# Kernel optimization log

Measured on AMD Instinct MI355X. Metric: run time of the kernel, lower is better.

Reference implementation:

```python
import jax, jax.numpy as jnp
import numpy as np
import math

BS, L, NNF, NEF = 8, 107, 17, 9
NH, EH, H3, NL, K = 128, 32, 32, 10, 3
PC, TL, TH, FF, NCLS = 32, 3, 8, 256, 3
D = NH + PC
HD = D // TH
RPG = 150
N = BS * L
E = BS * (2 * (L - 1) + RPG)
EPS = 1e-5


def _ln(z, g, b):
    m = z.mean(-1, keepdims=True)
    v = ((z - m) ** 2).mean(-1, keepdims=True)
    return (z - m) / jnp.sqrt(v + EPS) * g + b


def _gelu(z):
    return jax.nn.gelu(z, approximate=False)


def _forward(x, edge_attr, cheb_w, cheb_b, ee_w, ee_b, mlp_w1, mlp_b1, mlp_w2, mlp_b2,
             root_w, conv_b, ln_g, ln_b, attn_in_w, attn_in_b, attn_out_w, attn_out_b,
             ff_w1, ff_b1, ff_w2, ff_b2, tln1_g, tln1_b, tln2_g, tln2_b, lin_w, lin_b,
             seq_edge_index, edge_index):
    n = x.shape[0]
    # --- ChebConv (K=3, sym norm, lambda_max=2 -> L_hat = -D^-1/2 A D^-1/2) on seq edges ---
    ss, sd = seq_edge_index[0], seq_edge_index[1]
    deg = jax.ops.segment_sum(jnp.ones_like(ss, dtype=x.dtype), ss, num_segments=n)
    dinv = jnp.where(deg > 0, jax.lax.rsqrt(jnp.maximum(deg, 1e-12)), 0.0)
    w = -(dinv[ss] * dinv[sd])
    lap = lambda h: jax.ops.segment_sum(w[:, None] * h[ss], sd, num_segments=n)
    tx1 = lap(x)
    tx2 = 2.0 * lap(tx1) - x
    h = x @ cheb_w[0] + tx1 @ cheb_w[1] + tx2 @ cheb_w[2] + cheb_b

    # --- edge encoder ---
    ea = edge_attr @ ee_w + ee_b
    src, dst = edge_index[0], edge_index[1]

    # --- NNConv: per-edge weight W_e = MLP(ea) in R^{NHxNH}; gather-matmul-scatter ---
    def nnconv(h, l):
        we = ((ea @ mlp_w1[l] + mlp_b1[l]) @ mlp_w2[l] + mlp_b2[l]).reshape(-1, NH, NH)
        msg = jnp.einsum('ei,eio->eo', h[src], we)
        return jax.ops.segment_sum(msg, dst, num_segments=n) + h @ root_w[l] + conv_b[l]

    h = nnconv(h, 0)  # layers[0].conv applied directly (no residual)
    for l in range(1, NL):  # DeepGCNLayer res+: x + conv(gelu(LN(x)))
        h = h + nnconv(_gelu(_ln(h, ln_g[l], ln_b[l])), l)
    h = _gelu(_ln(h, ln_g[0], ln_b[0]))  # reuses layer 0's norm/act

    # --- sinusoidal position encoding (dim=PC), concat ---
    p = jnp.arange(L, dtype=x.dtype)[:, None]
    div = jnp.exp(jnp.arange(0, PC, 2, dtype=x.dtype) * (-math.log(10000.0) / PC))
    pos = jnp.zeros((L, PC), dtype=x.dtype)
    pos = pos.at[:, 0::2].set(jnp.sin(p * div)).at[:, 1::2].set(jnp.cos(p * div))

    t = jnp.concatenate([h.reshape(BS, L, NH), jnp.broadcast_to(pos, (BS, L, PC))], -1)

    # --- post-norm TransformerEncoder (relu FFN), vectorized over graphs ---
    scale = 1.0 / math.sqrt(HD)
    for l in range(TL):
        qkv = t @ attn_in_w[l] + attn_in_b[l]
        q, k, v = jnp.split(qkv, 3, axis=-1)
        q = q.reshape(BS, L, TH, HD)
        k = k.reshape(BS, L, TH, HD)
        v = v.reshape(BS, L, TH, HD)
        a = jax.nn.softmax(jnp.einsum('bqhd,bkhd->bhqk', q, k) * scale, axis=-1)
        o = jnp.einsum('bhqk,bkhd->bqhd', a, v).reshape(BS, L, D) @ attn_out_w[l] + attn_out_b[l]
        t = _ln(t + o, tln1_g[l], tln1_b[l])
        f = jax.nn.relu(t @ ff_w1[l] + ff_b1[l]) @ ff_w2[l] + ff_b2[l]
        t = _ln(t + f, tln2_g[l], tln2_b[l])

    return t.reshape(n, D) @ lin_w + lin_b


def setup_inputs():
    rng = np.random.default_rng(0)
    ks = iter(jax.random.split(jax.random.key(0), 40))
    # bidirectional sequence edges per graph + random pair edges
    base = np.arange(L - 1)
    s = np.concatenate([base, base + 1])
    d = np.concatenate([base + 1, base])
    off = (np.arange(BS) * L)[:, None]
    seq_src = (s[None] + off).ravel()
    seq_dst = (d[None] + off).ravel()
    r_src = (rng.integers(0, L, (BS, RPG)) + off).ravel()
    r_dst = (rng.integers(0, L, (BS, RPG)) + off).ravel()
    edge_index = jnp.asarray(np.stack([np.concatenate([seq_src, r_src]),
                                       np.concatenate([seq_dst, r_dst])]), dtype=jnp.int32)
    seq_edge_index = jnp.asarray(np.stack([seq_src, seq_dst]), dtype=jnp.int32)
    n_seq = seq_src.shape[0]

    def nrm(shape, sc=0.05):
        return jax.random.normal(next(ks), shape, dtype=jnp.float32) * sc

    x = jax.random.normal(next(ks), (N, NNF), dtype=jnp.float32)
    edge_attr = jax.random.normal(next(ks), (E, NEF), dtype=jnp.float32)
    col0 = jnp.concatenate([jnp.zeros((n_seq,), jnp.float32), jnp.ones((E - n_seq,), jnp.float32)])
    edge_attr = edge_attr.at[:, 0].set(col0)
    return {
        'x': x, 'edge_attr': edge_attr,
        'cheb_w': nrm((K, NNF, NH), 0.1), 'cheb_b': nrm((NH,), 0.02),
        'ee_w': nrm((NEF, EH), 0.1), 'ee_b': nrm((EH,), 0.02),
        'mlp_w1': nrm((NL, EH, H3), 0.1), 'mlp_b1': nrm((NL, H3), 0.02),
        'mlp_w2': nrm((NL, H3, NH * NH), 0.01), 'mlp_b2': nrm((NL, NH * NH), 0.01),
        'root_w': nrm((NL, NH, NH), 0.05), 'conv_b': nrm((NL, NH), 0.02),
        'ln_g': jnp.ones((NL, NH), jnp.float32), 'ln_b': jnp.zeros((NL, NH), jnp.float32),
        'attn_in_w': nrm((TL, D, 3 * D), 0.05), 'attn_in_b': nrm((TL, 3 * D), 0.02),
        'attn_out_w': nrm((TL, D, D), 0.05), 'attn_out_b': nrm((TL, D), 0.02),
        'ff_w1': nrm((TL, D, FF), 0.05), 'ff_b1': nrm((TL, FF), 0.02),
        'ff_w2': nrm((TL, FF, D), 0.05), 'ff_b2': nrm((TL, D), 0.02),
        'tln1_g': jnp.ones((TL, D), jnp.float32), 'tln1_b': jnp.zeros((TL, D), jnp.float32),
        'tln2_g': jnp.ones((TL, D), jnp.float32), 'tln2_b': jnp.zeros((TL, D), jnp.float32),
        'lin_w': nrm((D, NCLS), 0.05), 'lin_b': nrm((NCLS,), 0.02),
        'seq_edge_index': seq_edge_index, 'edge_index': edge_index,
    }


def reference(x, edge_attr, cheb_w, cheb_b, ee_w, ee_b, mlp_w1, mlp_b1, mlp_w2, mlp_b2,
              root_w, conv_b, ln_g, ln_b, attn_in_w, attn_in_b, attn_out_w, attn_out_b,
              ff_w1, ff_b1, ff_w2, ff_b2, tln1_g, tln1_b, tln2_g, tln2_b, lin_w, lin_b,
              seq_edge_index, edge_index):
    return _forward(x, edge_attr, cheb_w, cheb_b, ee_w, ee_b, mlp_w1, mlp_b1, mlp_w2, mlp_b2,
                    root_w, conv_b, ln_g, ln_b, attn_in_w, attn_in_b, attn_out_w, attn_out_b,
                    ff_w1, ff_b1, ff_w2, ff_b2, tln1_g, tln1_b, tln2_g, tln2_b, lin_w, lin_b,
                    seq_edge_index, edge_index)
```

## Files before the change

### kernel.cpp

```cpp
#include <hip/hip_runtime.h>
#include <hip/hip_bf16.h>
#include <math.h>

#define BSZ   8
#define LSEQ  107
#define NNF   17
#define NEF   9
#define NH    128
#define EHD   32
#define H3D   32
#define NLAY  10
#define PCD   32
#define TLAY  3
#define THD   8
#define FFD   256
#define NCLS  3
#define DD    160
#define HDD   20
#define NND   856
#define NPAD  896
#define NE    2896
#define CSTR  32
#define QKVP  512
#define PRJP  192
#define KTOT  1408
#define ALD2  1416

#define SB_CHEB 428
#define SB_PAD  (SB_CHEB)
#define SB_CSR1 (SB_PAD + 1)
#define SB_TPK  (SB_CSR1 + 1)
#define NTPK    171
#define SB_BIAS (SB_TPK + NTPK)
#define SB_WT   (SB_BIAS + 1)
#define NWT     160
#define SB_TOT  (SB_WT + NWT)

typedef __bf16 bf16;
typedef __bf16 bf16x2 __attribute__((ext_vector_type(2)));
typedef __bf16 bf16x8 __attribute__((ext_vector_type(8)));
typedef float  f32x4  __attribute__((ext_vector_type(4)));

__device__ __forceinline__ float geluf(float z) {
    return 0.5f * z * (1.0f + erff(z * 0.70710678118654752f));
}
__device__ __forceinline__ float wred(float v) {
    #pragma unroll
    for (int o = 32; o; o >>= 1) v += __shfl_xor(v, o, 64);
    return v;
}
__device__ __forceinline__ float dinv_path(int n) {
    return (n == 0 || n == LSEQ - 1) ? 1.0f : 0.70710678118654752f;
}

__global__ __launch_bounds__(256) void k_setup(
        const float* __restrict__ x, const float* __restrict__ cw,
        const float* __restrict__ cb, bf16* __restrict__ zA, bf16* __restrict__ zB,
        const float* __restrict__ eattr, const float* __restrict__ eew,
        const float* __restrict__ eeb, const float* __restrict__ w1,
        const float* __restrict__ b1,
        const float* __restrict__ w2, const float* __restrict__ b2,
        const float* __restrict__ rootw, bf16* __restrict__ bpk,
        const int* __restrict__ ei, int* __restrict__ deg,
        int* __restrict__ csrs, float* __restrict__ csrw,
        const float* __restrict__ ain_w, const float* __restrict__ aow,
        const float* __restrict__ ffw1, const float* __restrict__ ffw2,
        const float* __restrict__ ain_b, const float* __restrict__ aob,
        const float* __restrict__ ffb1, const float* __restrict__ ffb2,
        bf16* __restrict__ bqkv, bf16* __restrict__ bproj,
        bf16* __restrict__ bff1, bf16* __restrict__ bff2,
        float* __restrict__ tb_bias) {
    __shared__ __align__(16) char sm[24576];
    int blk = blockIdx.x, tid = threadIdx.x;
    if (blk < SB_CHEB) {
        float (*xs)[5][NNF] = (float (*)[5][NNF])sm;
        int s = tid >> 7, o = tid & 127;
        int n = blk * 2 + s;
        int g = n / LSEQ, i = n - g * LSEQ;
        if (o < 5 * NNF) {
            int k = o / NNF, f = o - k * NNF;
            int p = i - 2 + k; p = p < 0 ? 0 : (p > LSEQ - 1 ? LSEQ - 1 : p);
            xs[s][k][f] = x[(g * LSEQ + p) * NNF + f];
        }
        __syncthreads();
        float di  = dinv_path(i);
        float dm1 = dinv_path(i - 1 < 0 ? 0 : i - 1);
        float dp1 = dinv_path(i + 1 > LSEQ - 1 ? LSEQ - 1 : i + 1);
        float dm2 = dinv_path(i - 2 < 0 ? 0 : i - 2);
        float dp2 = dinv_path(i + 2 > LSEQ - 1 ? LSEQ - 1 : i + 2);
        float wmc = (i > 0)        ? -(dm1 * di) : 0.f;
        float wpc = (i < LSEQ - 1) ? -(dp1 * di) : 0.f;
        float wmm = (i - 1 > 0)        ? -(dm2 * dm1) : 0.f;
        float wpm = -(di * dm1);
        float wmp = -(di * dp1);
        float wpp = (i + 1 < LSEQ - 1) ? -(dp2 * dp1) : 0.f;
        float acc = cb[o];
        #pragma unroll
        for (int f = 0; f < NNF; ++f) {
            float xm2 = xs[s][0][f], xm1 = xs[s][1][f], x0 = xs[s][2][f],
                  xp1 = xs[s][3][f], xp2 = xs[s][4][f];
            float t1c = wmc * xm1 + wpc * xp1;
            float t1m = wmm * xm2 + wpm * x0;
            float t1p = wmp * x0 + wpp * xp2;
            float t2 = 2.f * (wmc * t1m + wpc * t1p) - x0;
            acc += x0 * cw[f * NH + o] + t1c * cw[(NNF + f) * NH + o]
                 + t2 * cw[(2 * NNF + f) * NH + o];
        }
        zA[n * NH + o] = (bf16)acc;
    } else if (blk == SB_PAD) {
        for (int i = tid; i < (NPAD - NND) * NH; i += 256) {
            zA[NND * NH + i] = (bf16)0.f;
            zB[NND * NH + i] = (bf16)0.f;
        }
    } else if (blk == SB_CSR1) {
        int* ldeg = (int*)sm;
        for (int i = tid; i < NND; i += 256) ldeg[i] = 0;
        __syncthreads();
        for (int e = tid; e < NE; e += 256) {
            int d = ei[NE + e];
            int slot = atomicAdd(&ldeg[d], 1);
            if (slot < CSTR) {
                int idx = d * CSTR + slot;
                csrs[idx] = ei[e];
                float* wp = csrw + (size_t)idx * 10;
                #pragma unroll
                for (int f = 0; f < NEF; ++f) wp[f] = eattr[e * NEF + f];
                wp[9] = 1.0f;
            }
        }
        __syncthreads();
        for (int i = tid; i < NND; i += 256) deg[i] = ldeg[i];
    } else if (blk < SB_BIAS) {
        bf16 (*tt)[65] = (bf16 (*)[65])sm;
        int v = blk - SB_TPK;
        int tl = v / 57, t = v % 57;
        const float* src; bf16* dst; int Kd, srcN, ct, kt;
        if (t < 24)      { ct = t & 7;  kt = t >> 3;          src = ain_w + (size_t)tl * DD * 3 * DD; srcN = 3 * DD; Kd = DD;  dst = bqkv  + (size_t)tl * QKVP * DD; }
        else if (t < 33) { int u = t - 24; ct = u % 3; kt = u / 3; src = aow + (size_t)tl * DD * DD;  srcN = DD;     Kd = DD;  dst = bproj + (size_t)tl * PRJP * DD; }
        else if (t < 45) { int u = t - 33; ct = u % 4; kt = u / 4; src = ffw1 + (size_t)tl * DD * FFD; srcN = FFD;   Kd = DD;  dst = bff1  + (size_t)tl * FFD * DD; }
        else             { int u = t - 45; ct = u % 3; kt = u / 3; src = ffw2 + (size_t)tl * FFD * DD; srcN = DD;    Kd = FFD; dst = bff2  + (size_t)tl * PRJP * FFD; }
        int cc = tid & 63, rr = tid >> 6;
        #pragma unroll
        for (int rep = 0; rep < 16; ++rep) {
            int kl = rep * 4 + rr;
            int k = kt * 64 + kl;
            int col = ct * 64 + cc;
            float val = (k < Kd && col < srcN) ? src[(size_t)k * srcN + col] : 0.f;
            tt[kl][cc] = (bf16)val;
        }
        __syncthreads();
        int k = kt * 64 + cc;
        if (k < Kd) {
            #pragma unroll
            for (int rep = 0; rep < 16; ++rep) {
                int c = rep * 4 + rr;
                dst[(size_t)(ct * 64 + c) * Kd + k] = tt[cc][c];
            }
        }
    } else if (blk == SB_BIAS) {
        for (int i = tid; i < 3 * 1152; i += 256) {
            int tl = i / 1152, r = i % 1152;
            float val;
            if (r < 512)      { val = (r < 480) ? ain_b[tl * 480 + r] : 0.f; }
            else if (r < 704) { int c = r - 512; val = (c < 160) ? aob[tl * 160 + c] : 0.f; }
            else if (r < 960) { int c = r - 704; val = ffb1[tl * 256 + c]; }
            else              { int c = r - 960; val = (c < 160) ? ffb2[tl * 160 + c] : 0.f; }
            tb_bias[i] = val;
        }
    } else {
        float* gw  = (float*)sm;
        bf16* ldsT = (bf16*)(sm + 2048);
        int v = blk - SB_WT;
        int l = v >> 4, chunk = v & 15;
        int io0 = chunk * 1024;
        for (int e = tid; e < 320; e += 256) {
            int f = e >> 5, j = e & 31;
            float acc;
            if (f < 9) {
                acc = 0.f;
                for (int m = 0; m < EHD; ++m)
                    acc += eew[f * EHD + m] * w1[(size_t)l * EHD * H3D + m * H3D + j];
            } else {
                acc = b1[l * H3D + j];
                for (int m = 0; m < EHD; ++m)
                    acc += eeb[m] * w1[(size_t)l * EHD * H3D + m * H3D + j];
            }
            gw[e] = acc;
        }
        __syncthreads();
        int io = io0 + tid * 4;
        const float* w2l = w2 + (size_t)l * 524288;
        float acc[10][4];
        float4 b2v = *(const float4*)(b2 + (size_t)l * 16384 + io);
        #pragma unroll
        for (int f = 0; f < 9; ++f) { acc[f][0] = 0.f; acc[f][1] = 0.f; acc[f][2] = 0.f; acc[f][3] = 0.f; }
        acc[9][0] = b2v.x; acc[9][1] = b2v.y; acc[9][2] = b2v.z; acc[9][3] = b2v.w;
        for (int j = 0; j < H3D; ++j) {
            float4 wv4 = *(const float4*)(w2l + (size_t)j * 16384 + io);
            #pragma unroll
            for (int f = 0; f < 10; ++f) {
                float gf = gw[f * 32 + j];
                acc[f][0] += gf * wv4.x; acc[f][1] += gf * wv4.y;
                acc[f][2] += gf * wv4.z; acc[f][3] += gf * wv4.w;
            }
        }
        int o4 = (tid & 31) * 4, il = tid >> 5;
        #pragma unroll
        for (int f = 0; f < 10; ++f)
            #pragma unroll
            for (int k = 0; k < 4; ++k)
                ldsT[(f * 128 + o4 + k) * 8 + il] = (bf16)acc[f][k];
        float4 rv = *(const float4*)(rootw + (size_t)l * 16384 + io);
        ldsT[(10 * 128 + o4 + 0) * 8 + il] = (bf16)rv.x;
        ldsT[(10 * 128 + o4 + 1) * 8 + il] = (bf16)rv.y;
        ldsT[(10 * 128 + o4 + 2) * 8 + il] = (bf16)rv.z;
        ldsT[(10 * 128 + o4 + 3) * 8 + il] = (bf16)rv.w;
        __syncthreads();
        if (tid < 128) {
            int o = tid;
            bf16* dst = bpk + (size_t)l * 128 * KTOT + (size_t)o * KTOT + chunk * 8;
            #pragma unroll
            for (int f = 0; f < 11; ++f) {
                bf16x8 val = *(bf16x8*)(ldsT + ((size_t)f * 128 + o) * 8);
                *(bf16x8*)(dst + f * 128) = val;
            }
        }
    }
}

__global__ __launch_bounds__(512) void k_layer(const bf16* __restrict__ zin,
                                               float* __restrict__ h,
                                               const bf16* __restrict__ bpkL,
                                               const float* __restrict__ conv_b,
                                               const float* __restrict__ lng,
                                               const float* __restrict__ lnb,
                                               bf16* __restrict__ zout,
                                               float* __restrict__ tbuf,
                                               const int* __restrict__ deg,
                                               const int* __restrict__ csrs,
                                               const float* __restrict__ csrw,
                                               int l) {
    __shared__ bf16 As[16][ALD2];
    __shared__ float outs[16][128];
    int tid = threadIdx.x, lane = tid & 63, wv = tid >> 6;
    int r0 = blockIdx.x * 16;
    for (int rr = 0; rr < 2; ++rr) {
        int r = wv * 2 + rr;
        int d = r0 + r;
        float acc[10][2];
        #pragma unroll
        for (int f = 0; f < 10; ++f) { acc[f][0] = 0.f; acc[f][1] = 0.f; }
        int dg = 0;
        if (d < NND) { dg = deg[d]; if (dg > CSTR) dg = CSTR; }
        for (int k = 0; k < dg; ++k) {
            int idx = d * CSTR + k;
            int s = csrs[idx];
            bf16x2 zz = *(const bf16x2*)(zin + (size_t)s * NH + 2 * lane);
            float z0 = (float)zz[0], z1 = (float)zz[1];
            const float* ww = csrw + (size_t)idx * 10;
            #pragma unroll
            for (int f = 0; f < 10; ++f) {
                float wf = ww[f];
                acc[f][0] += wf * z0;
                acc[f][1] += wf * z1;
            }
        }
        #pragma unroll
        for (int f = 0; f < 10; ++f) {
            bf16x2 av; av[0] = (bf16)acc[f][0]; av[1] = (bf16)acc[f][1];
            *(bf16x2*)(&As[r][f * 128 + 2 * lane]) = av;
        }
        bf16x2 zr = *(const bf16x2*)(zin + (size_t)d * NH + 2 * lane);
        *(bf16x2*)(&As[r][1280 + 2 * lane]) = zr;
    }
    __syncthreads();
    {
        int rA = lane & 15, q = lane >> 4, q8 = q * 8;
        const bf16* Af = &As[rA][0];
        const bf16* B0 = bpkL + (size_t)(wv * 16 + rA) * KTOT;
        f32x4 zf = {0.f, 0.f, 0.f, 0.f};
        f32x4 aA = zf, aB = zf;
        #pragma unroll 2
        for (int ks = 0; ks < 22; ++ks) {
            int kb = ks * 32 + q8;
            bf16x8 av = *(const bf16x8*)(Af + kb);
            bf16x8 b0 = *(const bf16x8*)(B0 + kb);
            aA = __builtin_amdgcn_mfma_f32_16x16x32_bf16(av, b0, aA, 0, 0, 0);
        }
        #pragma unroll 2
        for (int ks = 22; ks < 44; ++ks) {
            int kb = ks * 32 + q8;
            bf16x8 av = *(const bf16x8*)(Af + kb);
            bf16x8 b0 = *(const bf16x8*)(B0 + kb);
            aB = __builtin_amdgcn_mfma_f32_16x16x32_bf16(av, b0, aB, 0, 0, 0);
        }
        #pragma unroll
        for (int reg = 0; reg < 4; ++reg)
            outs[q * 4 + reg][wv * 16 + rA] = aA[reg] + aB[reg];
    }
    __syncthreads();
    for (int rr = 0; rr < 2; ++rr) {
        int r = wv * 2 + rr;
        int d = r0 + r;
        if (d >= NND) {
            if (l < NLAY - 1) {
                zout[d * NH + lane] = (bf16)0.f;
                zout[d * NH + lane + 64] = (bf16)0.f;
            }
            continue;
        }
        float v0 = outs[r][lane] + conv_b[l * NH + lane];
        float v1 = outs[r][lane + 64] + conv_b[l * NH + lane + 64];
        if (l > 0) {
            v0 += h[d * NH + lane];
            v1 += h[d * NH + lane + 64];
        }
        if (l < NLAY - 1) {
            h[d * NH + lane] = v0;
            h[d * NH + lane + 64] = v1;
        }
        float m = wred(v0 + v1) * (1.f / NH);
        float d0 = v0 - m, d1 = v1 - m;
        float var = wred(d0 * d0 + d1 * d1) * (1.f / NH);
        float rs = rsqrtf(var + 1e-5f);
        if (l < NLAY - 1) {
            int ln = l + 1;
            zout[d * NH + lane] = (bf16)geluf(d0 * rs * lng[ln * NH + lane] + lnb[ln * NH + lane]);
            zout[d * NH + lane + 64] = (bf16)geluf(d1 * rs * lng[ln * NH + lane + 64] + lnb[ln * NH + lane + 64]);
        } else {
            tbuf[(size_t)d * DD + lane] = geluf(d0 * rs * lng[lane] + lnb[lane]);
            tbuf[(size_t)d * DD + lane + 64] = geluf(d1 * rs * lng[lane + 64] + lnb[lane + 64]);
        }
    }
    if (l == NLAY - 1) {
        for (int idx = tid; idx < 16 * PCD; idx += 512) {
            int r = idx >> 5, pc = idx & 31;
            int d = r0 + r;
            if (d < NND) {
                int qq = d % LSEQ;
                float twoi = (float)(pc & ~1);
                float ang = (float)qq * expf(-twoi * 0.28782313662425572f);
                tbuf[(size_t)d * DD + NH + pc] = (pc & 1) ? cosf(ang) : sinf(ang);
            }
        }
    }
}

__global__ __launch_bounds__(256) void k_gmm(const float* __restrict__ A,
                                             const bf16* __restrict__ bp,
                                             const float* __restrict__ biasP,
                                             float* __restrict__ C,
                                             int ksteps, int K, int PW, int act) {
    int lane = threadIdx.x & 63, wv = threadIdx.x >> 6;
    int m0 = blockIdx.y * 64 + wv * 16;
    int ct = blockIdx.x;
    int r = lane & 15, q = lane >> 4, q8 = q * 8;
    const float* Arow = A + (size_t)(m0 + r) * K;
    const bf16* Bb = bp + ((size_t)ct * 64 + r) * K;
    f32x4 a0 = {0.f,0.f,0.f,0.f}, a1 = a0, a2 = a0, a3 = a0;
    for (int ks = 0; ks < ksteps; ++ks) {
        int kb = ks * 32 + q8;
        float4 f0 = *(const float4*)(Arow + kb);
        float4 f1 = *(const float4*)(Arow + kb + 4);
        bf16x8 av;
        av[0] = (bf16)f0.x; av[1] = (bf16)f0.y; av[2] = (bf16)f0.z; av[3] = (bf16)f0.w;
        av[4] = (bf16)f1.x; av[5] = (bf16)f1.y; av[6] = (bf16)f1.z; av[7] = (bf16)f1.w;
        bf16x8 b0 = *(const bf16x8*)(Bb + 0 * 16 * K + kb);
        bf16x8 b1 = *(const bf16x8*)(Bb + 1 * 16 * K + kb);
        bf16x8 b2 = *(const bf16x8*)(Bb + 2 * 16 * K + kb);
        bf16x8 b3 = *(const bf16x8*)(Bb + 3 * 16 * K + kb);
        a0 = __builtin_amdgcn_mfma_f32_16x16x32_bf16(av, b0, a0, 0, 0, 0);
        a1 = __builtin_amdgcn_mfma_f32_16x16x32_bf16(av, b1, a1, 0, 0, 0);
        a2 = __builtin_amdgcn_mfma_f32_16x16x32_bf16(av, b2, a2, 0, 0, 0);
        a3 = __builtin_amdgcn_mfma_f32_16x16x32_bf16(av, b3, a3, 0, 0, 0);
    }
    int cb = ct * 64;
    #pragma unroll
    for (int reg = 0; reg < 4; ++reg) {
        float* Crow = C + (size_t)(m0 + q * 4 + reg) * PW + cb;
        float v0 = a0[reg] + biasP[cb + 0 * 16 + r];
        float v1 = a1[reg] + biasP[cb + 1 * 16 + r];
        float v2 = a2[reg] + biasP[cb + 2 * 16 + r];
        float v3 = a3[reg] + biasP[cb + 3 * 16 + r];
        if (act) { v0 = fmaxf(v0, 0.f); v1 = fmaxf(v1, 0.f); v2 = fmaxf(v2, 0.f); v3 = fmaxf(v3, 0.f); }
        Crow[0 * 16 + r] = v0;
        Crow[1 * 16 + r] = v1;
        Crow[2 * 16 + r] = v2;
        Crow[3 * 16 + r] = v3;
    }
}

__global__ __launch_bounds__(512) void k_pln(const float* __restrict__ A,
                                             const bf16* __restrict__ bp,
                                             const float* __restrict__ biasP,
                                             int ksteps, int K,
                                             float* __restrict__ t,
                                             const float* __restrict__ g,
                                             const float* __restrict__ bvec,
                                             int tail,
                                             const bf16* __restrict__ tbp,
                                             const float* __restrict__ tbias_,
                                             float* __restrict__ tout,
                                             const float* __restrict__ lw,
                                             const float* __restrict__ lb,
                                             float* __restrict__ outp) {
    __shared__ float outs[16][PRJP];
    __shared__ bf16 Als[16][176];
    int tid = threadIdx.x, lane = tid & 63, wv = tid >> 6;
    int m0 = blockIdx.x * 16;
    if (wv < 6) {
        int r = lane & 15, q = lane >> 4, q8 = q * 8;
        const float* Arow = A + (size_t)(m0 + r) * K;
        int cb0 = wv * 32;
        const bf16* B0 = bp + ((size_t)(cb0 + r) * K);
        const bf16* B1 = bp + ((size_t)(cb0 + 16 + r) * K);
        f32x4 a0 = {0.f,0.f,0.f,0.f}, a1 = a0;
        for (int ks = 0; ks < ksteps; ++ks) {
            int kb = ks * 32 + q8;
            float4 f0 = *(const float4*)(Arow + kb);
            float4 f1 = *(const float4*)(Arow + kb + 4);
            bf16x8 av;
            av[0] = (bf16)f0.x; av[1] = (bf16)f0.y; av[2] = (bf16)f0.z; av[3] = (bf16)f0.w;
            av[4] = (bf16)f1.x; av[5] = (bf16)f1.y; av[6] = (bf16)f1.z; av[7] = (bf16)f1.w;
            bf16x8 b0 = *(const bf16x8*)(B0 + kb);
            bf16x8 b1 = *(const bf16x8*)(B1 + kb);
            a0 = __builtin_amdgcn_mfma_f32_16x16x32_bf16(av, b0, a0, 0, 0, 0);
            a1 = __builtin_amdgcn_mfma_f32_16x16x32_bf16(av, b1, a1, 0, 0, 0);
        }
        #pragma unroll
        for (int reg = 0; reg < 4; ++reg) {
            int rw = q * 4 + reg;
            outs[rw][cb0 + r] = a0[reg] + biasP[cb0 + r];
            outs[rw][cb0 + 16 + r] = a1[reg] + biasP[cb0 + 16 + r];
        }
    }
    __syncthreads();
    for (int rr = 0; rr < 2; ++rr) {
        int r = wv * 2 + rr;
        int d = m0 + r;
        if (d >= NND) continue;
        int c0 = lane, c1 = lane + 64, c2 = lane + 128;
        float v0 = outs[r][c0] + t[(size_t)d * DD + c0];
        float v1 = outs[r][c1] + t[(size_t)d * DD + c1];
        float v2 = (lane < 32) ? (outs[r][c2] + t[(size_t)d * DD + c2]) : 0.f;
        float m = wred(v0 + v1 + v2) * (1.f / DD);
        float d0 = v0 - m, d1 = v1 - m, d2 = (lane < 32) ? (v2 - m) : 0.f;
        float var = wred(d0 * d0 + d1 * d1 + d2 * d2) * (1.f / DD);
        float rs = rsqrtf(var + 1e-5f);
        float n0 = d0 * rs * g[c0] + bvec[c0];
        float n1 = d1 * rs * g[c1] + bvec[c1];
        float n2 = (lane < 32) ? (d2 * rs * g[c2] + bvec[c2]) : 0.f;
        t[(size_t)d * DD + c0] = n0;
        t[(size_t)d * DD + c1] = n1;
        if (lane < 32) t[(size_t)d * DD + c2] = n2;
        Als[r][c0] = (bf16)n0;
        Als[r][c1] = (bf16)n1;
        if (lane < 32) Als[r][c2] = (bf16)n2;
        if (tail == 0 && outp) {
            #pragma unroll
            for (int cls = 0; cls < NCLS; ++cls) {
                float part = n0 * lw[c0 * NCLS + cls] + n1 * lw[c1 * NCLS + cls]
                           + ((lane < 32) ? n2 * lw[c2 * NCLS + cls] : 0.f);
                float tot = wred(part);
                if (lane == 0) outp[d * NCLS + cls] = tot + lb[cls];
            }
        }
    }
    if (!tail) return;
    __syncthreads();
    {
        int PW = (tail == 1) ? FFD : QKVP;
        int ntile = (tail == 1) ? 2 : 4;
        int rA = lane & 15, q = lane >> 4, q8 = q * 8;
        for (int ctl = 0; ctl < ntile; ++ctl) {
            int cb = (wv * ntile + ctl) * 16;
            const bf16* Bb = tbp + ((size_t)cb + rA) * DD;
            f32x4 a0 = {0.f,0.f,0.f,0.f};
            #pragma unroll
            for (int ks = 0; ks < 5; ++ks) {
                int kb = ks * 32 + q8;
                bf16x8 av = *(const bf16x8*)(&Als[rA][0] + kb);
                bf16x8 b0 = *(const bf16x8*)(Bb + kb);
                a0 = __builtin_amdgcn_mfma_f32_16x16x32_bf16(av, b0, a0, 0, 0, 0);
            }
            #pragma unroll
            for (int reg = 0; reg < 4; ++reg) {
                float* Crow = tout + (size_t)(m0 + q * 4 + reg) * PW + cb;
                float v0 = a0[reg] + tbias_[cb + rA];
                if (tail == 1) v0 = fmaxf(v0, 0.f);
                Crow[rA] = v0;
            }
        }
    }
}

#define UPD4(ac, V) { ac.x = ac.x * corr + p * V.x; ac.y = ac.y * corr + p * V.y; \
                      ac.z = ac.z * corr + p * V.z; ac.w = ac.w * corr + p * V.w; }
__global__ __launch_bounds__(64) void k_attn(const float* __restrict__ qkv,
                                             float* __restrict__ aout) {
    __shared__ float4 Ks4[LSEQ * 5], Vs4[LSEQ * 5];
    int bh = blockIdx.x;
    int b = bh >> 3, hh = bh & 7;
    int tid = threadIdx.x;
    for (int i = tid; i < LSEQ * 5; i += 64) {
        int kq = i / 5, c4 = i - kq * 5;
        const float* rowp = qkv + (size_t)(b * LSEQ + kq) * QKVP + hh * HDD;
        Ks4[i] = ((const float4*)(rowp + DD))[c4];
        Vs4[i] = ((const float4*)(rowp + 2 * DD))[c4];
    }
    __syncthreads();
    int q = blockIdx.y * 64 + tid;
    if (q >= LSEQ) return;
    const float4* qp = (const float4*)(qkv + (size_t)(b * LSEQ + q) * QKVP + hh * HDD);
    float4 q0 = qp[0], q1 = qp[1], q2 = qp[2], q3 = qp[3], q4 = qp[4];
    const float scale = 0.22360679774997896f;
    float mx = -3.0e38f, sum = 0.f;
    float4 z = {0.f, 0.f, 0.f, 0.f};
    float4 ac0 = z, ac1 = z, ac2 = z, ac3 = z, ac4 = z;
    for (int k = 0; k < LSEQ; ++k) {
        const float4* kp = Ks4 + k * 5;
        float4 K0 = kp[0], K1 = kp[1], K2 = kp[2], K3 = kp[3], K4 = kp[4];
        float a0 = q0.x * K0.x + q0.y * K0.y + q0.z * K0.z + q0.w * K0.w;
        float a1 = q1.x * K1.x + q1.y * K1.y + q1.z * K1.z + q1.w * K1.w;
        float a2 = q2.x * K2.x + q2.y * K2.y + q2.z * K2.z + q2.w * K2.w;
        float a3 = q3.x * K3.x + q3.y * K3.y + q3.z * K3.z + q3.w * K3.w;
        float a4 = q4.x * K4.x + q4.y * K4.y + q4.z * K4.z + q4.w * K4.w;
        float s = (((a0 + a1) + (a2 + a3)) + a4) * scale;
        float mn = fmaxf(mx, s);
        float corr = __expf(mx - mn);
        float p = __expf(s - mn);
        mx = mn;
        sum = sum * corr + p;
        const float4* vp = Vs4 + k * 5;
        float4 V0 = vp[0], V1 = vp[1], V2 = vp[2], V3 = vp[3], V4 = vp[4];
        UPD4(ac0, V0); UPD4(ac1, V1); UPD4(ac2, V2); UPD4(ac3, V3); UPD4(ac4, V4);
    }
    float inv = 1.f / sum;
    float4* op = (float4*)(aout + (size_t)(b * LSEQ + q) * DD + hh * HDD);
    float4 o0 = {ac0.x * inv, ac0.y * inv, ac0.z * inv, ac0.w * inv};
    float4 o1 = {ac1.x * inv, ac1.y * inv, ac1.z * inv, ac1.w * inv};
    float4 o2 = {ac2.x * inv, ac2.y * inv, ac2.z * inv, ac2.w * inv};
    float4 o3 = {ac3.x * inv, ac3.y * inv, ac3.z * inv, ac3.w * inv};
    float4 o4 = {ac4.x * inv, ac4.y * inv, ac4.z * inv, ac4.w * inv};
    op[0] = o0; op[1] = o1; op[2] = o2; op[3] = o3; op[4] = o4;
}

extern "C" void kernel_launch(void* const* d_in, const int* in_sizes, int n_in,
                              void* d_out, int out_size, void* d_ws, size_t ws_size,
                              hipStream_t stream) {
    (void)in_sizes; (void)n_in; (void)out_size; (void)ws_size;
    const float* x      = (const float*)d_in[0];
    const float* eattr  = (const float*)d_in[1];
    const float* cheb_w = (const float*)d_in[2];
    const float* cheb_b = (const float*)d_in[3];
    const float* ee_w   = (const float*)d_in[4];
    const float* ee_b   = (const float*)d_in[5];
    const float* mlp_w1 = (const float*)d_in[6];
    const float* mlp_b1 = (const float*)d_in[7];
    const float* mlp_w2 = (const float*)d_in[8];
    const float* mlp_b2 = (const float*)d_in[9];
    const float* root_w = (const float*)d_in[10];
    const float* conv_b = (const float*)d_in[11];
    const float* ln_g   = (const float*)d_in[12];
    const float* ln_b   = (const float*)d_in[13];
    const float* ain_w  = (const float*)d_in[14];
    const float* ain_b  = (const float*)d_in[15];
    const float* aow    = (const float*)d_in[16];
    const float* aob    = (const float*)d_in[17];
    const float* ffw1   = (const float*)d_in[18];
    const float* ffb1   = (const float*)d_in[19];
    const float* ffw2   = (const float*)d_in[20];
    const float* ffb2   = (const float*)d_in[21];
    const float* t1g    = (const float*)d_in[22];
    const float* t1b    = (const float*)d_in[23];
    const float* t2g    = (const float*)d_in[24];
    const float* t2b    = (const float*)d_in[25];
    const float* lin_w  = (const float*)d_in[26];
    const float* lin_b  = (const float*)d_in[27];
    const int* ei       = (const int*)d_in[29];

    char* w = (char*)d_ws;
    size_t off = 0;
    auto alloc = [&](size_t bytes) -> void* {
        void* p = w + off;
        off += (bytes + 255) & ~(size_t)255;
        return p;
    };
    bf16*  bpk   = (bf16*)alloc((size_t)NLAY * 128 * KTOT * 2);
    float* h     = (float*)alloc((size_t)NND * NH * 4);
    bf16*  zA    = (bf16*)alloc((size_t)NPAD * NH * 2);
    bf16*  zB    = (bf16*)alloc((size_t)NPAD * NH * 2);
    float* tbuf  = (float*)alloc((size_t)NPAD * DD * 4);
    float* qkvC  = (float*)alloc((size_t)NPAD * QKVP * 4);
    float* abuf  = (float*)alloc((size_t)NPAD * DD * 4);
    float* f1    = (float*)alloc((size_t)NPAD * FFD * 4);
    int*   deg   = (int*)alloc((size_t)NND * 4);
    int*   csrs  = (int*)alloc((size_t)NND * CSTR * 4);
    float* csrw  = (float*)alloc((size_t)NND * CSTR * 10 * 4);
    bf16*  bqkv  = (bf16*)alloc((size_t)TLAY * QKVP * DD * 2);
    bf16*  bproj = (bf16*)alloc((size_t)TLAY * PRJP * DD * 2);
    bf16*  bff1  = (bf16*)alloc((size_t)TLAY * FFD * DD * 2);
    bf16*  bff2  = (bf16*)alloc((size_t)TLAY * PRJP * FFD * 2);
    float* tbias = (float*)alloc((size_t)TLAY * 1152 * 4);

    k_setup<<<SB_TOT, 256, 0, stream>>>(x, cheb_w, cheb_b, zA, zB,
                                        eattr, ee_w, ee_b, mlp_w1, mlp_b1,
                                        mlp_w2, mlp_b2, root_w, bpk,
                                        ei, deg, csrs, csrw,
                                        ain_w, aow, ffw1, ffw2,
                                        ain_b, aob, ffb1, ffb2,
                                        bqkv, bproj, bff1, bff2, tbias);

    bf16* zcur = zA;
    bf16* znxt = zB;
    for (int l = 0; l < NLAY; ++l) {
        k_layer<<<NPAD / 16, 512, 0, stream>>>(zcur, h, bpk + (size_t)l * 128 * KTOT,
                                               conv_b, ln_g, ln_b, znxt, tbuf,
                                               deg, csrs, csrw, l);
        bf16* tmp = zcur; zcur = znxt; znxt = tmp;
    }

    k_gmm<<<dim3(QKVP / 64, 14), 256, 0, stream>>>(tbuf, bqkv, tbias, qkvC, 5, DD, QKVP, 0);
    for (int tl = 0; tl < TLAY; ++tl) {
        const float* bb = tbias + (size_t)tl * 1152;
        k_attn<<<dim3(BSZ * THD, 2), 64, 0, stream>>>(qkvC, abuf);
        k_pln<<<NPAD / 16, 512, 0, stream>>>(abuf, bproj + (size_t)tl * PRJP * DD, bb + 512,
                                             5, DD, tbuf,
                                             t1g + (size_t)tl * DD, t1b + (size_t)tl * DD,
                                             1, bff1 + (size_t)tl * FFD * DD, bb + 704, f1,
                                             nullptr, nullptr, nullptr);
        int last = (tl == TLAY - 1);
        k_pln<<<NPAD / 16, 512, 0, stream>>>(f1, bff2 + (size_t)tl * PRJP * FFD, bb + 960,
                                             8, FFD, tbuf,
                                             t2g + (size_t)tl * DD, t2b + (size_t)tl * DD,
                                             last ? 0 : 2,
                                             last ? nullptr : bqkv + (size_t)(tl + 1) * QKVP * DD,
                                             last ? nullptr : tbias + (size_t)(tl + 1) * 1152,
                                             last ? nullptr : qkvC,
                                             last ? lin_w : nullptr,
                                             last ? lin_b : nullptr,
                                             last ? (float*)d_out : nullptr);
    }
}
```

Measured before the change: 466.6 us.

## Double k_layer block to 1024 threads with one row per wave and split-K MFMA

Each k_layer block now runs 16 waves instead of 8. Each wave gathers one destination row instead of two, and the MFMA stage splits the 44 K-steps between two waves per 16-column tile. The two partial results are written to separate shared buffers and summed in the epilogue. This halves the serial gather and matmul work per wave and adds latency hiding, at the cost of more shared memory and register pressure under 1024-thread launch bounds.

```diff
diff --git a/kernel.cpp b/kernel.cpp
--- a/kernel.cpp
+++ b/kernel.cpp
@@ -228,24 +228,24 @@
     }
 }
 
-__global__ __launch_bounds__(512) void k_layer(const bf16* __restrict__ zin,
-                                               float* __restrict__ h,
-                                               const bf16* __restrict__ bpkL,
-                                               const float* __restrict__ conv_b,
-                                               const float* __restrict__ lng,
-                                               const float* __restrict__ lnb,
-                                               bf16* __restrict__ zout,
-                                               float* __restrict__ tbuf,
-                                               const int* __restrict__ deg,
-                                               const int* __restrict__ csrs,
-                                               const float* __restrict__ csrw,
-                                               int l) {
+__global__ __launch_bounds__(1024) void k_layer(const bf16* __restrict__ zin,
+                                                float* __restrict__ h,
+                                                const bf16* __restrict__ bpkL,
+                                                const float* __restrict__ conv_b,
+                                                const float* __restrict__ lng,
+                                                const float* __restrict__ lnb,
+                                                bf16* __restrict__ zout,
+                                                float* __restrict__ tbuf,
+                                                const int* __restrict__ deg,
+                                                const int* __restrict__ csrs,
+                                                const float* __restrict__ csrw,
+                                                int l) {
     __shared__ bf16 As[16][ALD2];
-    __shared__ float outs[16][128];
+    __shared__ float outs[2][16][128];
     int tid = threadIdx.x, lane = tid & 63, wv = tid >> 6;
     int r0 = blockIdx.x * 16;
-    for (int rr = 0; rr < 2; ++rr) {
-        int r = wv * 2 + rr;
+    {
+        int r = wv;
         int d = r0 + r;
         float acc[10][2];
         #pragma unroll
@@ -276,64 +276,58 @@
     __syncthreads();
     {
         int rA = lane & 15, q = lane >> 4, q8 = q * 8;
+        int ct = wv >> 1, kh = wv & 1;
         const bf16* Af = &As[rA][0];
-        const bf16* B0 = bpkL + (size_t)(wv * 16 + rA) * KTOT;
-        f32x4 zf = {0.f, 0.f, 0.f, 0.f};
-        f32x4 aA = zf, aB = zf;
+        const bf16* B0 = bpkL + (size_t)(ct * 16 + rA) * KTOT;
+        f32x4 aA = {0.f, 0.f, 0.f, 0.f};
+        int ks0 = kh * 22;
         #pragma unroll 2
         for (int ks = 0; ks < 22; ++ks) {
-            int kb = ks * 32 + q8;
+            int kb = (ks0 + ks) * 32 + q8;
             bf16x8 av = *(const bf16x8*)(Af + kb);
             bf16x8 b0 = *(const bf16x8*)(B0 + kb);
             aA = __builtin_amdgcn_mfma_f32_16x16x32_bf16(av, b0, aA, 0, 0, 0);
         }
-        #pragma unroll 2
-        for (int ks = 22; ks < 44; ++ks) {
-            int kb = ks * 32 + q8;
-            bf16x8 av = *(const bf16x8*)(Af + kb);
-            bf16x8 b0 = *(const bf16x8*)(B0 + kb);
-            aB = __builtin_amdgcn_mfma_f32_16x16x32_bf16(av, b0, aB, 0, 0, 0);
-        }
         #pragma unroll
         for (int reg = 0; reg < 4; ++reg)
-            outs[q * 4 + reg][wv * 16 + rA] = aA[reg] + aB[reg];
+            outs[kh][q * 4 + reg][ct * 16 + rA] = aA[reg];
     }
     __syncthreads();
-    for (int rr = 0; rr < 2; ++rr) {
-        int r = wv * 2 + rr;
+    {
+        int r = wv;
         int d = r0 + r;
         if (d >= NND) {
             if (l < NLAY - 1) {
                 zout[d * NH + lane] = (bf16)0.f;
                 zout[d * NH + lane + 64] = (bf16)0.f;
             }
-            continue;
-        }
-        float v0 = outs[r][lane] + conv_b[l * NH + lane];
-        float v1 = outs[r][lane + 64] + conv_b[l * NH + lane + 64];
-        if (l > 0) {
-            v0 += h[d * NH + lane];
-            v1 += h[d * NH + lane + 64];
-        }
-        if (l < NLAY - 1) {
-            h[d * NH + lane] = v0;
-            h[d * NH + lane + 64] = v1;
-        }
-        float m = wred(v0 + v1) * (1.f / NH);
-        float d0 = v0 - m, d1 = v1 - m;
-        float var = wred(d0 * d0 + d1 * d1) * (1.f / NH);
-        float rs = rsqrtf(var + 1e-5f);
-        if (l < NLAY - 1) {
-            int ln = l + 1;
-            zout[d * NH + lane] = (bf16)geluf(d0 * rs * lng[ln * NH + lane] + lnb[ln * NH + lane]);
-            zout[d * NH + lane + 64] = (bf16)geluf(d1 * rs * lng[ln * NH + lane + 64] + lnb[ln * NH + lane + 64]);
         } else {
-            tbuf[(size_t)d * DD + lane] = geluf(d0 * rs * lng[lane] + lnb[lane]);
-            tbuf[(size_t)d * DD + lane + 64] = geluf(d1 * rs * lng[lane + 64] + lnb[lane + 64]);
+            float v0 = (outs[0][r][lane] + outs[1][r][lane]) + conv_b[l * NH + lane];
+            float v1 = (outs[0][r][lane + 64] + outs[1][r][lane + 64]) + conv_b[l * NH + lane + 64];
+            if (l > 0) {
+                v0 += h[d * NH + lane];
+                v1 += h[d * NH + lane + 64];
+            }
+            if (l < NLAY - 1) {
+                h[d * NH + lane] = v0;
+                h[d * NH + lane + 64] = v1;
+            }
+            float m = wred(v0 + v1) * (1.f / NH);
+            float d0 = v0 - m, d1 = v1 - m;
+            float var = wred(d0 * d0 + d1 * d1) * (1.f / NH);
+            float rs = rsqrtf(var + 1e-5f);
+            if (l < NLAY - 1) {
+                int ln = l + 1;
+                zout[d * NH + lane] = (bf16)geluf(d0 * rs * lng[ln * NH + lane] + lnb[ln * NH + lane]);
+                zout[d * NH + lane + 64] = (bf16)geluf(d1 * rs * lng[ln * NH + lane + 64] + lnb[ln * NH + lane + 64]);
+            } else {
+                tbuf[(size_t)d * DD + lane] = geluf(d0 * rs * lng[lane] + lnb[lane]);
+                tbuf[(size_t)d * DD + lane + 64] = geluf(d1 * rs * lng[lane + 64] + lnb[lane + 64]);
+            }
         }
     }
     if (l == NLAY - 1) {
-        for (int idx = tid; idx < 16 * PCD; idx += 512) {
+        for (int idx = tid; idx < 16 * PCD; idx += 1024) {
             int r = idx >> 5, pc = idx & 31;
             int d = r0 + r;
             if (d < NND) {
@@ -614,9 +608,9 @@
     bf16* zcur = zA;
     bf16* znxt = zB;
     for (int l = 0; l < NLAY; ++l) {
-        k_layer<<<NPAD / 16, 512, 0, stream>>>(zcur, h, bpk + (size_t)l * 128 * KTOT,
-                                               conv_b, ln_g, ln_b, znxt, tbuf,
-                                               deg, csrs, csrw, l);
+        k_layer<<<NPAD / 16, 1024, 0, stream>>>(zcur, h, bpk + (size_t)l * 128 * KTOT,
+                                                conv_b, ln_g, ln_b, znxt, tbuf,
+                                                deg, csrs, csrw, l);
         bf16* tmp = zcur; zcur = znxt; znxt = tmp;
     }
 
```

New measurement: 443.4 us, median of 2. 1.05x faster.
